# Performance work log

Measured on AMD Instinct MI355X. Metric: run time of the kernel, lower is better.

Reference implementation:

```python
import jax, jax.numpy as jnp
import numpy as np
from jax import lax

THRESHOLD = 1.0  # threshold_potential from __init__
STRIDE = (1, 1)
PADDING = 'SAME'


def setup_inputs() -> dict:
    key = jax.random.key(0)
    k1, k2, k3 = jax.random.split(key, 3)
    input_to_layer = jax.random.normal(k1, (1, 512, 512, 16), dtype=jnp.float32)
    weights = jax.random.normal(k2, (3, 3, 16, 64), dtype=jnp.float32)
    old_potentials = jax.random.normal(k3, (1, 512, 512, 64), dtype=jnp.float32)
    return {
        'input_to_layer': input_to_layer,
        'weights': weights,
        'old_potentials': old_potentials,
    }


def reference(input_to_layer, weights, old_potentials):
    # conv2d NHWC x HWIO -> NHWC, SAME padding, stride 1 (as tf.nn.conv2d)
    out_conv = lax.conv_general_dilated(
        input_to_layer, weights,
        window_strides=STRIDE, padding=PADDING,
        dimension_numbers=('NHWC', 'HWIO', 'NHWC'))
    # accumulate membrane potential, fused threshold -> spike + reset
    new_potentials = out_conv + old_potentials
    spiked = new_potentials >= THRESHOLD
    curr_spikes = spiked.astype(new_potentials.dtype)
    new_potentials = jnp.where(spiked, 0.0, new_potentials)
    # original returns spikes; new_potentials is the updated state
    return curr_spikes, new_potentials
```

## Files before the change

kernel.cpp:

```cpp
#include <hip/hip_runtime.h>


#define H 512
#define W 512
#define CI 16
#define CO 64
#define TX 32
#define TY 8
#define XT 34
#define YT 10
#define PIX_US 24
#define KS 152

typedef float v4f __attribute__((ext_vector_type(4)));
typedef float f32x4 __attribute__((ext_vector_type(4)));
typedef short short8 __attribute__((ext_vector_type(8)));
typedef unsigned int uint4v __attribute__((ext_vector_type(4)));

__device__ __forceinline__ unsigned int pack2bf(float f0, float f1) {
    unsigned u0 = __builtin_bit_cast(unsigned, f0);
    unsigned u1 = __builtin_bit_cast(unsigned, f1);
    u0 = (u0 + 0x7FFFu + ((u0 >> 16) & 1u)) >> 16;
    u1 = (u1 + 0x7FFFu + ((u1 >> 16) & 1u)) >> 16;
    return u0 | (u1 << 16);
}

__global__ __launch_bounds__(256, 4)
void snn_conv_mfma(const float* __restrict__ in,
                   const float* __restrict__ w,
                   const float* __restrict__ oldp,
                   float* __restrict__ out_spk,
                   float* __restrict__ out_pot)
{
    __shared__ unsigned short s_in[YT * XT * PIX_US];
    __shared__ unsigned short s_w[CO * KS];

    const int tid = threadIdx.x;
    const int bx = blockIdx.x & 15;
    const int by = blockIdx.x >> 4;
    const int tx0 = bx * TX, ty0 = by * TY;

    {
        const int n  = tid & 63;
        const int kq = tid >> 6;
        #pragma unroll
        for (int kk = 0; kk < 18; ++kk) {
            const int k = kq * 36 + kk * 2;
            const float f0 = w[k * CO + n];
            const float f1 = w[(k + 1) * CO + n];
            *(unsigned int*)&s_w[n * KS + k] = pack2bf(f0, f1);
        }
    }

    for (int idx = tid; idx < YT * XT; idx += 256) {
        const int ly = idx / XT, lx = idx - ly * XT;
        const int gy = ty0 + ly - 1, gx = tx0 + lx - 1;
        uint4v pk0, pk1;
        if ((unsigned)gy < H && (unsigned)gx < W) {
            const v4f* p = (const v4f*)(in + (gy * W + gx) * CI);
            v4f a = p[0], b = p[1], c = p[2], d = p[3];
            pk0 = (uint4v){pack2bf(a.x, a.y), pack2bf(a.z, a.w),
                           pack2bf(b.x, b.y), pack2bf(b.z, b.w)};
            pk1 = (uint4v){pack2bf(c.x, c.y), pack2bf(c.z, c.w),
                           pack2bf(d.x, d.y), pack2bf(d.z, d.w)};
        } else {
            pk0 = (uint4v)0u;
            pk1 = (uint4v)0u;
        }
        uint4v* dst = (uint4v*)&s_in[idx * PIX_US];
        dst[0] = pk0;
        dst[1] = pk1;
    }
    __syncthreads();

    const int lane = tid & 63;
    const int wv   = tid >> 6;
    const int r    = lane & 15;
    const int quad = lane >> 4;
    const int half = quad & 1;
    const int tsel = quad >> 1;

    f32x4 acc[4][4] = {};

    int pbase[4];
    #pragma unroll
    for (int pt = 0; pt < 4; ++pt) {
        const int rl = 2 * wv + (pt >> 1);
        const int xl = (pt & 1) * 16 + r;
        pbase[pt] = (rl * XT + xl) * PIX_US + half * 8;
    }

    const short8 zero8 = {0, 0, 0, 0, 0, 0, 0, 0};

    #pragma unroll
    for (int ks5 = 0; ks5 < 5; ++ks5) {
        const int t0 = ks5 * 2;
        const int t1 = (ks5 == 4) ? 8 : ks5 * 2 + 1;
        const int off0 = ((t0 / 3) * XT + (t0 % 3)) * PIX_US;
        const int off1 = ((t1 / 3) * XT + (t1 % 3)) * PIX_US;
        const int aoff = tsel ? off1 : off0;
        const int koff = (ks5 < 4) ? (ks5 * 32 + quad * 8) : (128 + half * 8);

        short8 wf[4];
        #pragma unroll
        for (int mt = 0; mt < 4; ++mt)
            wf[mt] = *(const short8*)&s_w[(mt * 16 + r) * KS + koff];

        short8 pf[4];
        #pragma unroll
        for (int pt = 0; pt < 4; ++pt) {
            short8 a = *(const short8*)&s_in[pbase[pt] + aoff];
            if (ks5 == 4) a = (quad >= 2) ? zero8 : a;
            pf[pt] = a;
        }

        #pragma unroll
        for (int mt = 0; mt < 4; ++mt)
            #pragma unroll
            for (int pt = 0; pt < 4; ++pt)
                acc[mt][pt] = __builtin_amdgcn_mfma_f32_16x16x32_bf16(
                    wf[mt], pf[pt], acc[mt][pt], 0, 0, 0);
    }

    #pragma unroll
    for (int pt = 0; pt < 4; ++pt) {
        const int gy = ty0 + 2 * wv + (pt >> 1);
        const int gx = tx0 + (pt & 1) * 16 + r;
        const int base0 = (gy * W + gx) * CO + quad * 4;
        #pragma unroll
        for (int mt = 0; mt < 4; ++mt) {
            const int idx = base0 + mt * 16;
            v4f old = *(const v4f*)(oldp + idx);
            const f32x4 a = acc[mt][pt];
            v4f spk, pot;
            #pragma unroll
            for (int c = 0; c < 4; ++c) {
                const float np = a[c] + old[c];
                const bool s = (np >= 1.0f);
                spk[c] = s ? 1.0f : 0.0f;
                pot[c] = s ? 0.0f : np;
            }
            *(v4f*)(out_spk + idx) = spk;
            *(v4f*)(out_pot + idx) = pot;
        }
    }
}

extern "C" void kernel_launch(void* const* d_in, const int* in_sizes, int n_in,
                              void* d_out, int out_size, void* d_ws, size_t ws_size,
                              hipStream_t stream) {
    const float* in   = (const float*)d_in[0];
    const float* w    = (const float*)d_in[1];
    const float* oldp = (const float*)d_in[2];
    float* out_spk = (float*)d_out;
    float* out_pot = out_spk + (size_t)H * W * CO;

    const int grid = (W / TX) * (H / TY);
    snn_conv_mfma<<<grid, 256, 0, stream>>>(in, w, oldp, out_spk, out_pot);
}
```

Before: 236.9 us.

## Prepack bf16 weights in a pre-kernel and prefetch old potentials before compute

Adds a small kernel that converts the weights to bf16 once in the workspace, so each conv block copies packed weights with vector loads instead of gathering and converting fp32 per block. The main kernel issues the old-potential loads for the first pixel tile before the barrier and MFMA loop, and double-buffers the remaining tiles in the epilogue to hide global-load latency. Launch bounds drop from 4 to 3 blocks per CU to leave room for the extra registers, which may lower occupancy. It also adds a second kernel launch and relies on the workspace being large enough.

Measured after the change: 221.9 us. -6.3%, faster.

```diff
diff --git a/kernel.cpp b/kernel.cpp
--- a/kernel.cpp
+++ b/kernel.cpp
@@ -25,9 +25,20 @@
     return u0 | (u1 << 16);
 }
 
-__global__ __launch_bounds__(256, 4)
+__global__ void conv_w_pack(const float* __restrict__ w,
+                            unsigned short* __restrict__ wbf) {
+    const int e = blockIdx.x * 256 + threadIdx.x;
+    const int k2 = e >> 6;
+    const int n  = e & 63;
+    const int k  = k2 * 2;
+    const float f0 = w[k * CO + n];
+    const float f1 = w[(k + 1) * CO + n];
+    *(unsigned int*)&wbf[n * KS + k] = pack2bf(f0, f1);
+}
+
+__global__ __launch_bounds__(256, 3)
 void snn_conv_mfma(const float* __restrict__ in,
-                   const float* __restrict__ w,
+                   const unsigned short* __restrict__ wbf,
                    const float* __restrict__ oldp,
                    float* __restrict__ out_spk,
                    float* __restrict__ out_pot)
@@ -41,14 +52,12 @@
     const int tx0 = bx * TX, ty0 = by * TY;
 
     {
-        const int n  = tid & 63;
-        const int kq = tid >> 6;
+        const uint4v* wsrc = (const uint4v*)wbf;
+        uint4v* wdst = (uint4v*)s_w;
         #pragma unroll
-        for (int kk = 0; kk < 18; ++kk) {
-            const int k = kq * 36 + kk * 2;
-            const float f0 = w[k * CO + n];
-            const float f1 = w[(k + 1) * CO + n];
-            *(unsigned int*)&s_w[n * KS + k] = pack2bf(f0, f1);
+        for (int i = 0; i < 5; ++i) {
+            const int idx = tid + i * 256;
+            if (idx < (CO * KS * 2) / 16) wdst[idx] = wsrc[idx];
         }
     }
 
@@ -71,7 +80,6 @@
         dst[0] = pk0;
         dst[1] = pk1;
     }
-    __syncthreads();
 
     const int lane = tid & 63;
     const int wv   = tid >> 6;
@@ -80,7 +88,19 @@
     const int half = quad & 1;
     const int tsel = quad >> 1;
 
-    f32x4 acc[4][4] = {};
+    int ebase[4];
+    #pragma unroll
+    for (int pt = 0; pt < 4; ++pt) {
+        const int gy = ty0 + 2 * wv + (pt >> 1);
+        const int gx = tx0 + (pt & 1) * 16 + r;
+        ebase[pt] = (gy * W + gx) * CO + quad * 4;
+    }
+    v4f oldb[2][4];
+    #pragma unroll
+    for (int mt = 0; mt < 4; ++mt)
+        oldb[0][mt] = *(const v4f*)(oldp + ebase[0] + mt * 16);
+
+    __syncthreads();
 
     int pbase[4];
     #pragma unroll
@@ -90,6 +110,7 @@
         pbase[pt] = (rl * XT + xl) * PIX_US + half * 8;
     }
 
+    f32x4 acc[4][4] = {};
     const short8 zero8 = {0, 0, 0, 0, 0, 0, 0, 0};
 
     #pragma unroll
@@ -124,13 +145,16 @@
 
     #pragma unroll
     for (int pt = 0; pt < 4; ++pt) {
-        const int gy = ty0 + 2 * wv + (pt >> 1);
-        const int gx = tx0 + (pt & 1) * 16 + r;
-        const int base0 = (gy * W + gx) * CO + quad * 4;
+        const int cur = pt & 1;
+        if (pt < 3) {
+            #pragma unroll
+            for (int mt = 0; mt < 4; ++mt)
+                oldb[1 - cur][mt] = *(const v4f*)(oldp + ebase[pt + 1] + mt * 16);
+        }
         #pragma unroll
         for (int mt = 0; mt < 4; ++mt) {
-            const int idx = base0 + mt * 16;
-            v4f old = *(const v4f*)(oldp + idx);
+            const int idx = ebase[pt] + mt * 16;
+            const v4f old = oldb[cur][mt];
             const f32x4 a = acc[mt][pt];
             v4f spk, pot;
             #pragma unroll
@@ -154,7 +178,9 @@
     const float* oldp = (const float*)d_in[2];
     float* out_spk = (float*)d_out;
     float* out_pot = out_spk + (size_t)H * W * CO;
+    unsigned short* wbf = (unsigned short*)d_ws;
 
+    conv_w_pack<<<18, 256, 0, stream>>>(w, wbf);
     const int grid = (W / TX) * (H / TY);
-    snn_conv_mfma<<<grid, 256, 0, stream>>>(in, w, oldp, out_spk, out_pot);
+    snn_conv_mfma<<<grid, 256, 0, stream>>>(in, wbf, oldp, out_spk, out_pot);
 }
```
